# Kernel tuning notes

Measured on AMD Instinct MI355X. Metric: run time of the kernel, lower is better.

The kernel has to match this reference:

```python
import jax, jax.numpy as jnp
import numpy as np

B, NQ, NV, DIM, HEADS, K = 2, 2048, 2048, 256, 8, 8
HD = DIM // HEADS
HID = 4 * DIM
SCALE = HD ** -0.5
EPS = 1e-5


def setup_inputs() -> dict:
    key = jax.random.key(0)
    ks = jax.random.split(key, 40)
    r = lambda i, s: jax.random.normal(ks[i], s, jnp.float32) * 0.02
    inp = {
        'q': jax.random.normal(ks[0], (B, NQ, DIM), jnp.float32),
        'v': jax.random.normal(ks[1], (B, NV, DIM), jnp.float32),
        'q_pos': jax.random.normal(ks[2], (B, NQ, 3), jnp.float32),
        'v_pos': jax.random.normal(ks[3], (B, NV, 3), jnp.float32),
        'self_knn_index': jax.random.randint(ks[4], (B, NQ, K), 0, NQ, jnp.int32),
        'cross_knn_index': jax.random.randint(ks[5], (B, NQ, K), 0, NV, jnp.int32),
        # LayerNorms (gamma=1, beta=0)
        'norm1_g': jnp.ones(DIM), 'norm1_b': jnp.zeros(DIM),
        'normq_g': jnp.ones(DIM), 'normq_b': jnp.zeros(DIM),
        'normv_g': jnp.ones(DIM), 'normv_b': jnp.zeros(DIM),
        'norm2_g': jnp.ones(DIM), 'norm2_b': jnp.zeros(DIM),
        # self-attention (qkv_bias=False), proj has bias
        'sa_qkv_w': r(6, (DIM, 3 * DIM)),
        'sa_proj_w': r(7, (DIM, DIM)), 'sa_proj_b': jnp.zeros(DIM),
        # cross-attention: q proj and kv proj (no bias), out proj with bias
        'ca_q_w': r(8, (DIM, DIM)),
        'ca_kv_w': r(9, (DIM, 2 * DIM)),
        'ca_proj_w': r(10, (DIM, DIM)), 'ca_proj_b': jnp.zeros(DIM),
        # MLP
        'fc1_w': r(11, (DIM, HID)), 'fc1_b': jnp.zeros(HID),
        'fc2_w': r(12, (HID, DIM)), 'fc2_b': jnp.zeros(DIM),
        # kNN maps
        'knn_w': r(13, (2 * DIM, DIM)), 'knn_b': jnp.zeros(DIM),
        'merge_w': r(14, (2 * DIM, DIM)), 'merge_b': jnp.zeros(DIM),
        'knnx_w': r(15, (2 * DIM, DIM)), 'knnx_b': jnp.zeros(DIM),
        'mergex_w': r(16, (2 * DIM, DIM)), 'mergex_b': jnp.zeros(DIM),
    }
    return inp


def _ln(x, g, b):
    m = x.mean(-1, keepdims=True)
    var = x.var(-1, keepdims=True)
    return (x - m) / jnp.sqrt(var + EPS) * g + b


def _heads(x):  # [B,N,DIM] -> [B,H,N,HD]
    Bx, N, _ = x.shape
    return x.reshape(Bx, N, HEADS, HD).transpose(0, 2, 1, 3)


def _attend(qh, kh, vh, proj_w, proj_b):
    a = jax.nn.softmax(jnp.einsum('bhqd,bhkd->bhqk', qh, kh) * SCALE, axis=-1)
    o = jnp.einsum('bhqk,bhkd->bhqd', a, vh)
    Bx, _, N, _ = o.shape
    o = o.transpose(0, 2, 1, 3).reshape(Bx, N, DIM)
    return o @ proj_w + proj_b


_gather = jax.vmap(lambda pts, idx: pts[idx])  # ([N,D],[Nq,K]) -> [Nq,K,D]


def _knn_feature(qn, vn, idx):  # gather -> diff/cat -> [B,Nq,K,2D]
    local = _gather(vn, idx)                      # [B,Nq,K,D]
    qe = qn[:, :, None, :]                        # [B,Nq,1,D]
    return jnp.concatenate([local - qe, jnp.broadcast_to(qe, local.shape)], -1)


def reference(q, v, q_pos, v_pos, self_knn_index, cross_knn_index,
              norm1_g, norm1_b, normq_g, normq_b, normv_g, normv_b,
              norm2_g, norm2_b, sa_qkv_w, sa_proj_w, sa_proj_b,
              ca_q_w, ca_kv_w, ca_proj_w, ca_proj_b,
              fc1_w, fc1_b, fc2_w, fc2_b,
              knn_w, knn_b, merge_w, merge_b,
              knnx_w, knnx_b, mergex_w, mergex_b):
    # ---- self-attention block with self-kNN branch ----
    nq = _ln(q, norm1_g, norm1_b)
    qkv = nq @ sa_qkv_w
    qh, kh, vh = (_heads(t) for t in jnp.split(qkv, 3, axis=-1))
    sa_out = _attend(qh, kh, vh, sa_proj_w, sa_proj_b)
    f = _knn_feature(nq, nq, self_knn_index)
    knn_out = jax.nn.leaky_relu(f @ knn_w + knn_b, 0.2).max(axis=-2)
    q1 = jnp.concatenate([sa_out, knn_out], -1) @ merge_w + merge_b
    q = q + q1
    # ---- cross-attention block with cross-kNN branch ----
    nq2 = _ln(q, normq_g, normq_b)
    nv = _ln(v, normv_g, normv_b)
    qh = _heads(nq2 @ ca_q_w)
    kh, vh = (_heads(t) for t in jnp.split(nv @ ca_kv_w, 2, axis=-1))
    ca_out = _attend(qh, kh, vh, ca_proj_w, ca_proj_b)
    f = _knn_feature(nq2, nv, cross_knn_index)
    knnx_out = jax.nn.leaky_relu(f @ knnx_w + knnx_b, 0.2).max(axis=-2)
    q2 = jnp.concatenate([ca_out, knnx_out], -1) @ mergex_w + mergex_b
    q = q + q2
    # ---- MLP block ----
    h = _ln(q, norm2_g, norm2_b)
    h = jax.nn.gelu(h @ fc1_w + fc1_b, approximate=False)
    q = q + (h @ fc2_w + fc2_b)
    return q
```

## Files before the change

### kernel.cpp

```cpp
#include <hip/hip_runtime.h>
#include <math.h>

#define NQC   2048
#define NKVC  2048
#define DIMC  256
#define SCALEF 0.2550348810731232f

typedef short bfrag __attribute__((ext_vector_type(8)));
typedef float ffrag __attribute__((ext_vector_type(4)));
typedef unsigned short us8 __attribute__((ext_vector_type(8)));

__device__ __forceinline__ float gelu_exact(float x) {
    return 0.5f * x * (1.0f + erff(x * 0.70710678118654752f));
}
__device__ __forceinline__ unsigned short f2bf(float f) {
    union { float f; unsigned u; } v; v.f = f;
    unsigned r = v.u + 0x7FFFu + ((v.u >> 16) & 1u);
    return (unsigned short)(r >> 16);
}
__device__ __forceinline__ float bf2f(unsigned short u) {
    union { unsigned u; float f; } v; v.u = ((unsigned)u) << 16;
    return v.f;
}
__device__ __forceinline__ float fexp2(float x) {
    float r; asm("v_exp_f32 %0, %1" : "=v"(r) : "v"(x)); return r;
}
__device__ __forceinline__ unsigned cvt_pk_bf16(float lo, float hi) {
    unsigned r; asm("v_cvt_pk_bf16_f32 %0, %1, %2" : "=v"(r) : "v"(lo), "v"(hi));
    return r;
}

__device__ __forceinline__ void ln_row(
    const float* __restrict__ x, const float* __restrict__ g,
    const float* __restrict__ b, unsigned short* __restrict__ y, int row)
{
    int lane = threadIdx.x & 63;
    const float* xr = x + (size_t)row * DIMC + lane * 4;
    float4 vv = *(const float4*)xr;
    float s  = vv.x + vv.y + vv.z + vv.w;
    float sq = vv.x*vv.x + vv.y*vv.y + vv.z*vv.z + vv.w*vv.w;
    #pragma unroll
    for (int off = 32; off >= 1; off >>= 1) {
        s  += __shfl_xor(s, off);
        sq += __shfl_xor(sq, off);
    }
    float mean = s * (1.0f/DIMC);
    float inv  = rsqrtf(sq * (1.0f/DIMC) - mean*mean + 1e-5f);
    float4 gg = *(const float4*)(g + lane*4);
    float4 bb = *(const float4*)(b + lane*4);
    ushort4 o;
    o.x = f2bf((vv.x - mean) * inv * gg.x + bb.x);
    o.y = f2bf((vv.y - mean) * inv * gg.y + bb.y);
    o.z = f2bf((vv.z - mean) * inv * gg.z + bb.z);
    o.w = f2bf((vv.w - mean) * inv * gg.w + bb.w);
    *(ushort4*)(y + (size_t)row * DIMC + lane * 4) = o;
}

__global__ __launch_bounds__(256) void prep_w(
    const float* __restrict__ qkv, const float* __restrict__ knn,
    const float* __restrict__ proj, const float* __restrict__ merge,
    const float* __restrict__ caq, const float* __restrict__ knnx,
    const float* __restrict__ cakv, const float* __restrict__ projx,
    const float* __restrict__ mergex, const float* __restrict__ fc1,
    const float* __restrict__ fc2, unsigned short* __restrict__ dst,
    const float* __restrict__ lx, const float* __restrict__ lg,
    const float* __restrict__ lb, unsigned short* __restrict__ ly,
    const float* __restrict__ vx, const float* __restrict__ vg,
    const float* __restrict__ vb, unsigned short* __restrict__ vy,
    const float* __restrict__ pb1, const float* __restrict__ mb1, float* __restrict__ bf1o,
    const float* __restrict__ pbx, const float* __restrict__ mbx, float* __restrict__ bfxo)
{
    __shared__ unsigned short T[64][72];
    int blk = blockIdx.x, tid = threadIdx.x;
    if (blk >= 2528) {
        const float* bp = (blk == 2528) ? pb1 : pbx;
        const float* Wm = (blk == 2528) ? merge : mergex;
        const float* bm = (blk == 2528) ? mb1 : mbx;
        float* o        = (blk == 2528) ? bf1o : bfxo;
        int m = tid;
        float acc = bm[m];
        for (int k = 0; k < 256; ++k) acc += bp[k] * Wm[(size_t)k * 256 + m];
        o[m] = acc;
        return;
    }
    if (blk >= 1504) {
        ln_row(vx, vg, vb, vy, (blk - 1504) * 4 + (tid >> 6));
        return;
    }
    if (blk >= 480) {
        ln_row(lx, lg, lb, ly, (blk - 480) * 4 + (tid >> 6));
        return;
    }
    if (blk >= 352) {
        int l = blk - 352;
        const float* s; unsigned short* d;
        if (l < 64) { s = proj;  d = dst + 327680; }
        else        { s = projx; d = dst + 851968; l -= 64; }
        int e = (l * 256 + tid) * 4;
        float4 v = *(const float4*)(s + e);
        ushort4 o;
        o.x = f2bf(v.x); o.y = f2bf(v.y); o.z = f2bf(v.z); o.w = f2bf(v.w);
        *(ushort4*)(d + e) = o;
        return;
    }
    int t = blk;
    const float* src; const float* src2 = nullptr; int sN;
    unsigned short* dp; int dK; float scale = 1.0f; int n0, k0;
    if (t < 48)       { src = qkv;          sN = 768;  dp = dst;           dK = 256;
                        n0 = (t % 12) * 64; k0 = (t / 12) * 64; if (n0 < 256) scale = SCALEF; }
    else if (t < 64)  { int u = t - 48;  src = knn;          sN = 256; dp = dst + 196608; dK = 256;
                        n0 = (u & 3) * 64; k0 = (u >> 2) * 64; }
    else if (t < 80)  { int u = t - 64;  src = knn + 65536;  src2 = knn; sN = 256; dp = dst + 262144; dK = 256;
                        n0 = (u & 3) * 64; k0 = (u >> 2) * 64; }
    else if (t < 112) { int u = t - 80;  src = merge;        sN = 256; dp = dst + 393216; dK = 512;
                        n0 = (u & 3) * 64; k0 = (u >> 2) * 64; }
    else if (t < 128) { int u = t - 112; src = caq;          sN = 256; dp = dst + 524288; dK = 256;
                        n0 = (u & 3) * 64; k0 = (u >> 2) * 64; scale = SCALEF; }
    else if (t < 144) { int u = t - 128; src = knnx + 65536; src2 = knnx; sN = 256; dp = dst + 589824; dK = 256;
                        n0 = (u & 3) * 64; k0 = (u >> 2) * 64; }
    else if (t < 176) { int u = t - 144; src = cakv;         sN = 512; dp = dst + 655360; dK = 256;
                        n0 = (u & 7) * 64; k0 = (u >> 3) * 64; }
    else if (t < 192) { int u = t - 176; src = knnx;         sN = 256; dp = dst + 786432; dK = 256;
                        n0 = (u & 3) * 64; k0 = (u >> 2) * 64; }
    else if (t < 224) { int u = t - 192; src = mergex;       sN = 256; dp = dst + 917504; dK = 512;
                        n0 = (u & 3) * 64; k0 = (u >> 2) * 64; }
    else if (t < 288) { int u = t - 224; src = fc1;          sN = 1024; dp = dst + 1048576; dK = 256;
                        n0 = (u & 15) * 64; k0 = (u >> 4) * 64; }
    else              { int u = t - 288; src = fc2;          sN = 256; dp = dst + 1310720; dK = 1024;
                        n0 = (u & 3) * 64; k0 = (u >> 2) * 64; }
    int r = tid >> 2, c0 = (tid & 3) * 16;
    float va[16];
    {
        const float* sp = src + (size_t)(k0 + r) * sN + n0 + c0;
        float4 f0 = *(const float4*)(sp);
        float4 f1 = *(const float4*)(sp + 4);
        float4 f2 = *(const float4*)(sp + 8);
        float4 f3 = *(const float4*)(sp + 12);
        va[0]=f0.x; va[1]=f0.y; va[2]=f0.z;  va[3]=f0.w;
        va[4]=f1.x; va[5]=f1.y; va[6]=f1.z;  va[7]=f1.w;
        va[8]=f2.x; va[9]=f2.y; va[10]=f2.z; va[11]=f2.w;
        va[12]=f3.x; va[13]=f3.y; va[14]=f3.z; va[15]=f3.w;
        if (src2) {
            const float* s2 = src2 + (size_t)(k0 + r) * sN + n0 + c0;
            float4 h0 = *(const float4*)(s2);
            float4 h1 = *(const float4*)(s2 + 4);
            float4 h2 = *(const float4*)(s2 + 8);
            float4 h3 = *(const float4*)(s2 + 12);
            va[0]-=h0.x; va[1]-=h0.y; va[2]-=h0.z;  va[3]-=h0.w;
            va[4]-=h1.x; va[5]-=h1.y; va[6]-=h1.z;  va[7]-=h1.w;
            va[8]-=h2.x; va[9]-=h2.y; va[10]-=h2.z; va[11]-=h2.w;
            va[12]-=h3.x; va[13]-=h3.y; va[14]-=h3.z; va[15]-=h3.w;
        }
    }
    #pragma unroll
    for (int i = 0; i < 16; ++i) T[c0 + i][r] = f2bf(va[i] * scale);
    __syncthreads();
    {
        int n = tid >> 2, kk = (tid & 3) * 16;
        unsigned short* d = dp + (size_t)(n0 + n) * dK + k0 + kk;
        *(us8*)d       = *(const us8*)&T[n][kk];
        *(us8*)(d + 8) = *(const us8*)&T[n][kk + 8];
    }
}

template<int ACT, int RESID, int OUTBF>
__device__ __forceinline__ void gemm_body(
    const unsigned short* __restrict__ A, int lda,
    const unsigned short* __restrict__ Wt,
    const float* __restrict__ bias,
    const float* __restrict__ resid, int ldr,
    void* __restrict__ Cp, int ldc, int Kc, int row0, int col0,
    unsigned short (* __restrict__ Alds)[72],
    unsigned short (* __restrict__ Wlds)[72])
{
    const int tid = threadIdx.x;
    const int wid = tid >> 6, lane = tid & 63;
    const int lm = lane & 15, quad = lane >> 4;
    const int wr = wid >> 1, wc = wid & 1;
    const int ar = tid >> 2, ac = (tid & 3) * 16;
    const unsigned short* Ag = A  + (size_t)(row0 + ar) * lda + ac;
    const unsigned short* Wg = Wt + (size_t)(col0 + ar) * Kc  + ac;

    us8 a0 = *(const us8*)Ag;
    us8 a1 = *(const us8*)(Ag + 8);
    us8 w0 = *(const us8*)Wg;
    us8 w1 = *(const us8*)(Wg + 8);

    ffrag acc[2][2];
    #pragma unroll
    for (int mi = 0; mi < 2; ++mi)
        #pragma unroll
        for (int ni = 0; ni < 2; ++ni)
            acc[mi][ni] = (ffrag){0.f, 0.f, 0.f, 0.f};

    for (int k0 = 0;;) {
        __syncthreads();
        *(us8*)&Alds[ar][ac]   = a0;
        *(us8*)&Alds[ar][ac+8] = a1;
        *(us8*)&Wlds[ar][ac]   = w0;
        *(us8*)&Wlds[ar][ac+8] = w1;
        __syncthreads();
        k0 += 64;
        if (k0 < Kc) {
            a0 = *(const us8*)(Ag + k0);
            a1 = *(const us8*)(Ag + k0 + 8);
            w0 = *(const us8*)(Wg + k0);
            w1 = *(const us8*)(Wg + k0 + 8);
        }
        #pragma unroll
        for (int kc = 0; kc < 2; ++kc) {
            bfrag af[2], bw[2];
            #pragma unroll
            for (int mi = 0; mi < 2; ++mi)
                af[mi] = *(const bfrag*)&Alds[wr*32 + mi*16 + lm][kc*32 + quad*8];
            #pragma unroll
            for (int ni = 0; ni < 2; ++ni)
                bw[ni] = *(const bfrag*)&Wlds[wc*32 + ni*16 + lm][kc*32 + quad*8];
            #pragma unroll
            for (int mi = 0; mi < 2; ++mi)
                #pragma unroll
                for (int ni = 0; ni < 2; ++ni)
                    acc[mi][ni] = __builtin_amdgcn_mfma_f32_16x16x32_bf16(
                        af[mi], bw[ni], acc[mi][ni], 0, 0, 0);
        }
        if (k0 >= Kc) break;
    }
    #pragma unroll
    for (int mi = 0; mi < 2; ++mi) {
        #pragma unroll
        for (int ni = 0; ni < 2; ++ni) {
            int gr = row0 + wr*32 + mi*16 + quad*4;
            int gc = col0 + wc*32 + ni*16 + lm;
            float bv = bias ? bias[gc] : 0.f;
            #pragma unroll
            for (int r = 0; r < 4; ++r) {
                float o = acc[mi][ni][r] + bv;
                if (ACT == 1) o = gelu_exact(o);
                if (RESID) o += resid[(size_t)(gr + r) * ldr + gc];
                if (OUTBF) ((unsigned short*)Cp)[(size_t)(gr + r) * ldc + gc] = f2bf(o);
                else       ((float*)Cp)[(size_t)(gr + r) * ldc + gc] = o;
            }
        }
    }
}

template<int ACT, int RESID, int OUTBF>
__global__ __launch_bounds__(256) void gemm64(
    const unsigned short* __restrict__ A, int lda,
    const unsigned short* __restrict__ Wt,
    const float* __restrict__ bias,
    const float* __restrict__ resid, int ldr,
    void* __restrict__ Cp, int ldc, int Kc)
{
    __shared__ unsigned short Alds[64][72];
    __shared__ unsigned short Wlds[64][72];
    gemm_body<ACT,RESID,OUTBF>(A, lda, Wt, bias, resid, ldr, Cp, ldc, Kc,
                               blockIdx.y * 64, blockIdx.x * 64, Alds, Wlds);
}

__global__ __launch_bounds__(256) void gemm_qkv_fold(
    const unsigned short* __restrict__ XB, const unsigned short* __restrict__ WT1,
    unsigned short* __restrict__ A1,
    const unsigned short* __restrict__ WTmerge, const unsigned short* __restrict__ projbf,
    unsigned short* __restrict__ WTf1,
    const unsigned short* __restrict__ WTmergex, const unsigned short* __restrict__ projxbf,
    unsigned short* __restrict__ WTfx)
{
    __shared__ unsigned short Alds[64][72];
    __shared__ unsigned short Wlds[64][72];
    const unsigned short *A, *Wt; unsigned short* C;
    int lda, ldc, row0, col0;
    if (blockIdx.y >= 64) {
        if (blockIdx.x >= 16) return;
        row0 = (blockIdx.x >> 2) * 64; col0 = (blockIdx.x & 3) * 64;
        lda = 512; ldc = 256;
        if (blockIdx.y == 64) { A = WTmerge;  Wt = projbf;  C = WTf1; }
        else                  { A = WTmergex; Wt = projxbf; C = WTfx; }
    } else {
        A = XB; Wt = WT1; C = A1; lda = 256; ldc = 1280;
        row0 = blockIdx.y * 64; col0 = blockIdx.x * 64;
    }
    gemm_body<0,0,1>(A, lda, Wt, nullptr, nullptr, 0, C, ldc, 256, row0, col0, Alds, Wlds);
}

template<int ACT, int RESID, int OUTBF>
__global__ __launch_bounds__(512) void gemm64x8(
    const unsigned short* __restrict__ A, int lda,
    const unsigned short* __restrict__ Wt,
    const float* __restrict__ bias,
    const float* __restrict__ resid, int ldr,
    void* __restrict__ Cp, int ldc, int Kc)
{
    __shared__ unsigned short Alds[2][64][72];
    __shared__ unsigned short Wlds[2][64][72];
    __shared__ float Red[64][68];
    const int tid = threadIdx.x;
    const int g = tid >> 8;
    const int t = tid & 255;
    const int wid2 = (tid >> 6) & 3, lane = tid & 63;
    const int lm = lane & 15, quad = lane >> 4;
    const int wr = wid2 >> 1, wc = wid2 & 1;
    const int row0 = blockIdx.y * 64, col0 = blockIdx.x * 64;
    const int ar = t >> 2, ac = (t & 3) * 16;
    const int KH = Kc >> 1;
    const unsigned short* Ag = A  + (size_t)(row0 + ar) * lda + g * KH + ac;
    const unsigned short* Wg = Wt + (size_t)(col0 + ar) * Kc  + g * KH + ac;

    us8 a0 = *(const us8*)Ag;
    us8 a1 = *(const us8*)(Ag + 8);
    us8 w0 = *(const us8*)Wg;
    us8 w1 = *(const us8*)(Wg + 8);

    ffrag acc[2][2];
    #pragma unroll
    for (int mi = 0; mi < 2; ++mi)
        #pragma unroll
        for (int ni = 0; ni < 2; ++ni)
            acc[mi][ni] = (ffrag){0.f, 0.f, 0.f, 0.f};

    for (int k0 = 0;;) {
        __syncthreads();
        *(us8*)&Alds[g][ar][ac]   = a0;
        *(us8*)&Alds[g][ar][ac+8] = a1;
        *(us8*)&Wlds[g][ar][ac]   = w0;
        *(us8*)&Wlds[g][ar][ac+8] = w1;
        __syncthreads();
        k0 += 64;
        if (k0 < KH) {
            a0 = *(const us8*)(Ag + k0);
            a1 = *(const us8*)(Ag + k0 + 8);
            w0 = *(const us8*)(Wg + k0);
            w1 = *(const us8*)(Wg + k0 + 8);
        }
        #pragma unroll
        for (int kc = 0; kc < 2; ++kc) {
            bfrag af[2], bw[2];
            #pragma unroll
            for (int mi = 0; mi < 2; ++mi)
                af[mi] = *(const bfrag*)&Alds[g][wr*32 + mi*16 + lm][kc*32 + quad*8];
            #pragma unroll
            for (int ni = 0; ni < 2; ++ni)
                bw[ni] = *(const bfrag*)&Wlds[g][wc*32 + ni*16 + lm][kc*32 + quad*8];
            #pragma unroll
            for (int mi = 0; mi < 2; ++mi)
                #pragma unroll
                for (int ni = 0; ni < 2; ++ni)
                    acc[mi][ni] = __builtin_amdgcn_mfma_f32_16x16x32_bf16(
                        af[mi], bw[ni], acc[mi][ni], 0, 0, 0);
        }
        if (k0 >= KH) break;
    }
    __syncthreads();
    if (g == 1) {
        #pragma unroll
        for (int mi = 0; mi < 2; ++mi)
            #pragma unroll
            for (int ni = 0; ni < 2; ++ni) {
                int lr = wr*32 + mi*16 + quad*4;
                int lc = wc*32 + ni*16 + lm;
                #pragma unroll
                for (int r = 0; r < 4; ++r)
                    Red[lr + r][lc] = acc[mi][ni][r];
            }
    }
    __syncthreads();
    if (g == 0) {
        #pragma unroll
        for (int mi = 0; mi < 2; ++mi) {
            #pragma unroll
            for (int ni = 0; ni < 2; ++ni) {
                int lr = wr*32 + mi*16 + quad*4;
                int lc = wc*32 + ni*16 + lm;
                int gr = row0 + lr;
                int gc = col0 + lc;
                float bv = bias ? bias[gc] : 0.f;
                #pragma unroll
                for (int r = 0; r < 4; ++r) {
                    float o = acc[mi][ni][r] + Red[lr + r][lc] + bv;
                    if (ACT == 1) o = gelu_exact(o);
                    if (RESID) o += resid[(size_t)(gr + r) * ldr + gc];
                    if (OUTBF) ((unsigned short*)Cp)[(size_t)(gr + r) * ldc + gc] = f2bf(o);
                    else       ((float*)Cp)[(size_t)(gr + r) * ldc + gc] = o;
                }
            }
        }
    }
}

__global__ __launch_bounds__(512) void gemm_mln(
    const unsigned short* __restrict__ Op, const float* __restrict__ Lp,
    const unsigned short* __restrict__ Akn,
    const unsigned short* __restrict__ Wat,
    const unsigned short* __restrict__ Wkn,
    const float* __restrict__ bias,
    const float* __restrict__ resid,
    float* __restrict__ Cp,
    const float* __restrict__ lng, const float* __restrict__ lnb,
    unsigned short* __restrict__ ln_out)
{
    __shared__ unsigned short Wlds[256][72];
    __shared__ unsigned short Alds[16][72];
    __shared__ float OutT[16][268];
    const int tid = threadIdx.x;
    const int wid = tid >> 6, lane = tid & 63;
    const int lm = lane & 15, quad = lane >> 4;
    const int row0 = blockIdx.x * 16;
    const int wn = tid >> 1, wk = (tid & 1) * 32;
    const int ar = tid >> 3, ac = (tid & 7) * 8;

    const unsigned short* O0 = Op + (size_t)(row0 + ar) * 256 + ac;
    const unsigned short* O1 = Op + (size_t)(4096 + row0 + ar) * 256 + ac;
    const float* L0 = Lp + (size_t)(row0 + ar) * 8;
    const float* L1 = Lp + (size_t)(4096 + row0 + ar) * 8;
    const unsigned short* Ak = Akn + (size_t)(row0 + ar) * 512 + ac;

    us8 aReg, wv0, wv1, wv2, wv3;
    if (tid < 128) {
        us8 x = *(const us8*)O0;
        us8 y = *(const us8*)O1;
        float li = 1.0f / (L0[ac >> 5] + L1[ac >> 5]);
        #pragma unroll
        for (int i = 0; i < 8; ++i)
            aReg[i] = f2bf((bf2f(x[i]) + bf2f(y[i])) * li);
    }
    {
        const unsigned short* Wg = Wat + (size_t)wn * 256 + wk;
        wv0 = *(const us8*)Wg;        wv1 = *(const us8*)(Wg + 8);
        wv2 = *(const us8*)(Wg + 16); wv3 = *(const us8*)(Wg + 24);
    }

    ffrag acc[2];
    acc[0] = (ffrag){0.f, 0.f, 0.f, 0.f};
    acc[1] = (ffrag){0.f, 0.f, 0.f, 0.f};

    for (int k0 = 0;;) {
        __syncthreads();
        if (tid < 128) *(us8*)&Alds[ar][ac] = aReg;
        *(us8*)&Wlds[wn][wk]      = wv0;
        *(us8*)&Wlds[wn][wk + 8]  = wv1;
        *(us8*)&Wlds[wn][wk + 16] = wv2;
        *(us8*)&Wlds[wn][wk + 24] = wv3;
        __syncthreads();
        k0 += 64;
        if (k0 < 512) {
            if (tid < 128) {
                if (k0 < 256) {
                    us8 x = *(const us8*)(O0 + k0);
                    us8 y = *(const us8*)(O1 + k0);
                    float li = 1.0f / (L0[(k0 + ac) >> 5] + L1[(k0 + ac) >> 5]);
                    #pragma unroll
                    for (int i = 0; i < 8; ++i)
                        aReg[i] = f2bf((bf2f(x[i]) + bf2f(y[i])) * li);
                } else {
                    aReg = *(const us8*)(Ak + (k0 - 256));
                }
            }
            const unsigned short* Wg = (k0 < 256)
                ? Wat + (size_t)wn * 256 + k0 + wk
                : Wkn + (size_t)wn * 512 + (k0 - 256) + wk;
            wv0 = *(const us8*)Wg;        wv1 = *(const us8*)(Wg + 8);
            wv2 = *(const us8*)(Wg + 16); wv3 = *(const us8*)(Wg + 24);
        }
        #pragma unroll
        for (int kc = 0; kc < 2; ++kc) {
            bfrag af = *(const bfrag*)&Alds[lm][kc*32 + quad*8];
            #pragma unroll
            for (int ni = 0; ni < 2; ++ni) {
                bfrag bw = *(const bfrag*)&Wlds[wid*32 + ni*16 + lm][kc*32 + quad*8];
                acc[ni] = __builtin_amdgcn_mfma_f32_16x16x32_bf16(
                    af, bw, acc[ni], 0, 0, 0);
            }
        }
        if (k0 >= 512) break;
    }
    #pragma unroll
    for (int ni = 0; ni < 2; ++ni) {
        int gc = wid*32 + ni*16 + lm;
        float bv = bias[gc];
        #pragma unroll
        for (int r = 0; r < 4; ++r) {
            int lr = quad*4 + r;
            float o = acc[ni][r] + bv + resid[(size_t)(row0 + lr) * 256 + gc];
            Cp[(size_t)(row0 + lr) * 256 + gc] = o;
            OutT[lr][gc] = o;
        }
    }
    __syncthreads();
    #pragma unroll
    for (int rr0 = 0; rr0 < 2; ++rr0) {
        int rr = wid * 2 + rr0;
        float4 vv = *(const float4*)&OutT[rr][lane * 4];
        float s  = vv.x + vv.y + vv.z + vv.w;
        float sq = vv.x*vv.x + vv.y*vv.y + vv.z*vv.z + vv.w*vv.w;
        #pragma unroll
        for (int off = 32; off >= 1; off >>= 1) {
            s  += __shfl_xor(s, off);
            sq += __shfl_xor(sq, off);
        }
        float mean = s * (1.0f/DIMC);
        float inv  = rsqrtf(sq * (1.0f/DIMC) - mean*mean + 1e-5f);
        float4 gg = *(const float4*)(lng + lane*4);
        float4 bb = *(const float4*)(lnb + lane*4);
        ushort4 o;
        o.x = f2bf((vv.x - mean) * inv * gg.x + bb.x);
        o.y = f2bf((vv.y - mean) * inv * gg.y + bb.y);
        o.z = f2bf((vv.z - mean) * inv * gg.z + bb.z);
        o.w = f2bf((vv.w - mean) * inv * gg.w + bb.w);
        *(ushort4*)(ln_out + (size_t)(row0 + rr) * 256 + lane * 4) = o;
    }
}

__global__ __launch_bounds__(256) void gemm64_dual(
    const unsigned short* __restrict__ XB,
    const unsigned short* __restrict__ NVB,
    const unsigned short* __restrict__ WT2,
    const unsigned short* __restrict__ WT3,
    unsigned short* __restrict__ A2,
    unsigned short* __restrict__ A3)
{
    __shared__ unsigned short Alds[64][72];
    __shared__ unsigned short Wlds[64][72];
    const unsigned short* A; const unsigned short* Wt;
    unsigned short* C; int ldc, col0;
    if (blockIdx.x < 8) { A = XB;  Wt = WT2; C = A2; ldc = 512; col0 = blockIdx.x * 64; }
    else                { A = NVB; Wt = WT3; C = A3; ldc = 768; col0 = (blockIdx.x - 8) * 64; }
    gemm_body<0,0,1>(A, 256, Wt, nullptr, nullptr, 0, C, ldc, 256,
                     blockIdx.y * 64, col0, Alds, Wlds);
}

__global__ __launch_bounds__(256) void attn_gather(
    const unsigned short* __restrict__ Qp, int ldq,
    const unsigned short* __restrict__ Kp, int ldk,
    const unsigned short* __restrict__ Vp, int ldv,
    unsigned short* __restrict__ Op, float* __restrict__ Lp,
    const unsigned short* __restrict__ P, int ldp,
    const unsigned short* __restrict__ Base, int ldb,
    const float* __restrict__ gbias, const int* __restrict__ idx,
    unsigned short* __restrict__ gout, int ldgo)
{
    __shared__ unsigned short Klds[64][40];
    __shared__ __align__(16) unsigned short Vt[32][72];
    __shared__ __align__(16) unsigned short Plds[4][16][72];
    int tid = threadIdx.x, wid = tid >> 6, lane = tid & 63;

    if (blockIdx.z >= 4) {
        int gbid = blockIdx.x + 32 * (blockIdx.y + 8 * (blockIdx.z - 4));
        int q = gbid * 4 + wid;
        int b = q >> 11;
        int c = lane * 4;
        ushort4 bu = *(const ushort4*)(Base + (size_t)q * ldb + c);
        float4 bi = *(const float4*)(gbias + c);
        float bsx = bf2f(bu.x) + bi.x, bsy = bf2f(bu.y) + bi.y;
        float bsz = bf2f(bu.z) + bi.z, bsw = bf2f(bu.w) + bi.w;
        float4 acc = make_float4(-3e38f, -3e38f, -3e38f, -3e38f);
        const int* ip = idx + (size_t)q * 8;
        #pragma unroll
        for (int k = 0; k < 8; ++k) {
            int j = ip[k];
            ushort4 pu = *(const ushort4*)(P + ((size_t)(b * NKVC + j)) * ldp + c);
            float t;
            t = bsx + bf2f(pu.x); t = t > 0.f ? t : 0.2f * t; acc.x = fmaxf(acc.x, t);
            t = bsy + bf2f(pu.y); t = t > 0.f ? t : 0.2f * t; acc.y = fmaxf(acc.y, t);
            t = bsz + bf2f(pu.z); t = t > 0.f ? t : 0.2f * t; acc.z = fmaxf(acc.z, t);
            t = bsw + bf2f(pu.w); t = t > 0.f ? t : 0.2f * t; acc.w = fmaxf(acc.w, t);
        }
        ushort4 o;
        o.x = f2bf(acc.x); o.y = f2bf(acc.y); o.z = f2bf(acc.z); o.w = f2bf(acc.w);
        *(ushort4*)(gout + (size_t)q * ldgo + c) = o;
        return;
    }

    int zc = blockIdx.z, bb = zc >> 1, ck = zc & 1;
    int h = blockIdx.y;
    int hoff = h * 32;
    int lm = lane & 15, quad = lane >> 4;
    size_t qbase  = (size_t)bb * NQC;
    size_t kvbase = (size_t)bb * NKVC;
    int q0 = blockIdx.x * 64 + wid * 16;

    bfrag aq = *(const bfrag*)(Qp + (qbase + q0 + lm) * (size_t)ldq + hoff + quad * 8);

    float l_r[4] = {0.f, 0.f, 0.f, 0.f};
    ffrag oacc[2];
    oacc[0] = (ffrag){0.f, 0.f, 0.f, 0.f};
    oacc[1] = (ffrag){0.f, 0.f, 0.f, 0.f};

    const int kkey = tid >> 2, kd0 = (tid & 3) * 8;
    const int vkey = tid & 63, vd0 = (tid >> 6) * 8;
    const int vcol = ((vkey & 15) << 2) | (vkey >> 4);
    const unsigned short* kg0 = Kp + (kvbase + kkey) * (size_t)ldk + hoff + kd0;
    const unsigned short* vg0 = Vp + (kvbase + vkey) * (size_t)ldv + hoff + vd0;

    for (int kt = ck * 16; kt < ck * 16 + 16; ++kt) {
        us8 kv = *(const us8*)(kg0 + (size_t)kt * 64 * ldk);
        us8 vv = *(const us8*)(vg0 + (size_t)kt * 64 * ldv);
        __syncthreads();
        *(us8*)&Klds[kkey][kd0] = kv;
        #pragma unroll
        for (int i = 0; i < 8; ++i) Vt[vd0 + i][vcol] = vv[i];
        __syncthreads();

        ffrag sacc[4];
        #pragma unroll
        for (int t = 0; t < 4; ++t) {
            bfrag bk = *(const bfrag*)&Klds[t*16 + lm][quad * 8];
            sacc[t] = __builtin_amdgcn_mfma_f32_16x16x32_bf16(
                aq, bk, (ffrag){0.f,0.f,0.f,0.f}, 0, 0, 0);
        }

        #pragma unroll
        for (int r = 0; r < 4; ++r) {
            float p0 = fexp2(sacc[0][r]), p1 = fexp2(sacc[1][r]);
            float p2 = fexp2(sacc[2][r]), p3 = fexp2(sacc[3][r]);
            l_r[r] += (p0 + p1) + (p2 + p3);
            unsigned u0 = cvt_pk_bf16(p0, p1);
            unsigned u1 = cvt_pk_bf16(p2, p3);
            *(uint2*)&Plds[wid][quad*4 + r][lm << 2] = make_uint2(u0, u1);
        }
        asm volatile("s_waitcnt lgkmcnt(0)" ::: "memory");

        #pragma unroll
        for (int kc = 0; kc < 2; ++kc) {
            bfrag ap = *(const bfrag*)&Plds[wid][lm][kc*32 + quad*8];
            #pragma unroll
            for (int nt = 0; nt < 2; ++nt) {
                bfrag bv = *(const bfrag*)&Vt[nt*16 + lm][kc*32 + quad*8];
                oacc[nt] = __builtin_amdgcn_mfma_f32_16x16x32_bf16(
                    ap, bv, oacc[nt], 0, 0, 0);
            }
        }
    }
    #pragma unroll
    for (int nt = 0; nt < 2; ++nt)
        #pragma unroll
        for (int r = 0; r < 4; ++r)
            Op[((size_t)ck * 4096 + qbase + q0 + quad*4 + r) * 256 + hoff + nt*16 + lm]
                = f2bf(oacc[nt][r]);
    #pragma unroll
    for (int r = 0; r < 4; ++r) {
        float l = l_r[r];
        l += __shfl_xor(l, 1);
        l += __shfl_xor(l, 2);
        l += __shfl_xor(l, 4);
        l += __shfl_xor(l, 8);
        if (lm == 0)
            Lp[((size_t)ck * 4096 + qbase + q0 + quad*4 + r) * 8 + h] = l;
    }
}

extern "C" void kernel_launch(void* const* d_in, const int* in_sizes, int n_in,
                              void* d_out, int out_size, void* d_ws, size_t ws_size,
                              hipStream_t stream) {
    const float* q_in   = (const float*)d_in[0];
    const float* v_in   = (const float*)d_in[1];
    const int*   idx_s  = (const int*)d_in[4];
    const int*   idx_x  = (const int*)d_in[5];
    const float* n1g = (const float*)d_in[6],  *n1b = (const float*)d_in[7];
    const float* nqg = (const float*)d_in[8],  *nqb = (const float*)d_in[9];
    const float* nvg = (const float*)d_in[10], *nvb = (const float*)d_in[11];
    const float* n2g = (const float*)d_in[12], *n2b = (const float*)d_in[13];
    const float* sa_qkv_w  = (const float*)d_in[14];
    const float* sa_proj_w = (const float*)d_in[15];
    const float* sa_proj_b = (const float*)d_in[16];
    const float* ca_q_w    = (const float*)d_in[17];
    const float* ca_kv_w   = (const float*)d_in[18];
    const float* ca_proj_w = (const float*)d_in[19];
    const float* ca_proj_b = (const float*)d_in[20];
    const float* fc1_w = (const float*)d_in[21], *fc1_b = (const float*)d_in[22];
    const float* fc2_w = (const float*)d_in[23], *fc2_b = (const float*)d_in[24];
    const float* knn_w   = (const float*)d_in[25], *knn_b   = (const float*)d_in[26];
    const float* merge_w = (const float*)d_in[27], *merge_b = (const float*)d_in[28];
    const float* knnx_w  = (const float*)d_in[29], *knnx_b  = (const float*)d_in[30];
    const float* mergex_w = (const float*)d_in[31], *mergex_b = (const float*)d_in[32];
    float* out = (float*)d_out;

    unsigned short* A1      = (unsigned short*)d_ws;
    unsigned short* A2      = A1;
    unsigned short* A3      = A1 + (size_t)4096 * 512;
    unsigned short* Hb      = A1;
    unsigned short* KN      = A1 + (size_t)4096 * 1280;
    unsigned short* CC      = KN;
    unsigned short* XB      = CC + (size_t)4096 * 512;
    unsigned short* NVB     = XB + (size_t)4096 * 256;
    unsigned short* WT      = NVB + (size_t)4096 * 256;
    unsigned short* WT1     = WT;
    unsigned short* projbf  = WT + 327680;
    unsigned short* WTmerge = WT + 393216;
    unsigned short* WT2     = WT + 524288;
    unsigned short* WT3     = WT + 655360;
    unsigned short* projxbf = WT + 851968;
    unsigned short* WTmergex= WT + 917504;
    unsigned short* WTfc1   = WT + 1048576;
    unsigned short* WTfc2   = WT + 1310720;
    unsigned short* Opart   = WT + 1572864;
    float* Lpart = (float*)(Opart + (size_t)2 * 4096 * 256);
    unsigned short* WTf1 = (unsigned short*)(Lpart + (size_t)2 * 4096 * 8);
    unsigned short* WTfx = WTf1 + 65536;
    float* bf1 = (float*)(WTfx + 65536);
    float* bfx = bf1 + 256;

    dim3 blk(256), blk8(512);
    dim3 gAG(NQC / 64, 8, 8);

    prep_w<<<dim3(2530), blk, 0, stream>>>(sa_qkv_w, knn_w, sa_proj_w, merge_w,
        ca_q_w, knnx_w, ca_kv_w, ca_proj_w, mergex_w, fc1_w, fc2_w, WT,
        q_in, n1g, n1b, XB,
        v_in, nvg, nvb, NVB,
        sa_proj_b, merge_b, bf1,
        ca_proj_b, mergex_b, bfx);

    gemm_qkv_fold<<<dim3(20,66), blk, 0, stream>>>(XB, WT1, A1,
        WTmerge, projbf, WTf1, WTmergex, projxbf, WTfx);
    attn_gather<<<gAG, blk, 0, stream>>>(A1, 1280, A1+256, 1280, A1+512, 1280,
        Opart, Lpart, A1+768, 1280, A1+1024, 1280, knn_b, idx_s, CC+256, 512);
    gemm_mln<<<dim3(256), blk8, 0, stream>>>(Opart, Lpart, CC+256,
        WTf1, WTmerge+256, bf1, q_in, out, nqg, nqb, XB);

    gemm64_dual<<<dim3(20,64), blk, 0, stream>>>(XB, NVB, WT2, WT3, A2, A3);
    attn_gather<<<gAG, blk, 0, stream>>>(A2, 512, A3, 768, A3+256, 768,
        Opart, Lpart, A3+512, 768, A2+256, 512, knnx_b, idx_x, CC+256, 512);
    gemm_mln<<<dim3(256), blk8, 0, stream>>>(Opart, Lpart, CC+256,
        WTfx, WTmergex+256, bfx, out, out, n2g, n2b, XB);

    gemm64<1,0,1><<<dim3(16,64), blk, 0, stream>>>(XB, 256, WTfc1,
        fc1_b, nullptr, 0, Hb, 1024, 256);
    gemm64x8<0,1,0><<<dim3(4,64), blk8, 0, stream>>>(Hb, 1024, WTfc2,
        fc2_b, out, 256, out, 256, 1024);
}
```

Before: 235.6 us.

## Process two query tiles per wave in attention to reuse K/V LDS tiles

Each wave now handles 32 queries (two 16-row MFMA tiles) instead of 16, so each block covers 128 queries. Every K/V tile staged in shared memory feeds twice as many MFMAs, which halves K/V global loads and barriers per query. Attention blocks with blockIdx.x >= 16 exit early, while the grid shape stays 32 wide so the gather branch keeps its indexing. The cost is more registers per wave, a larger P buffer in LDS, and half as many attention blocks, which lowers parallelism.

```diff
diff --git a/kernel.cpp b/kernel.cpp
--- a/kernel.cpp
+++ b/kernel.cpp
@@ -540,7 +540,7 @@
 {
     __shared__ unsigned short Klds[64][40];
     __shared__ __align__(16) unsigned short Vt[32][72];
-    __shared__ __align__(16) unsigned short Plds[4][16][72];
+    __shared__ __align__(16) unsigned short Plds[4][2][16][72];
     int tid = threadIdx.x, wid = tid >> 6, lane = tid & 63;
 
     if (blockIdx.z >= 4) {
@@ -570,20 +570,26 @@
         return;
     }
 
+    if (blockIdx.x >= 16) return;
     int zc = blockIdx.z, bb = zc >> 1, ck = zc & 1;
     int h = blockIdx.y;
     int hoff = h * 32;
     int lm = lane & 15, quad = lane >> 4;
     size_t qbase  = (size_t)bb * NQC;
     size_t kvbase = (size_t)bb * NKVC;
-    int q0 = blockIdx.x * 64 + wid * 16;
-
-    bfrag aq = *(const bfrag*)(Qp + (qbase + q0 + lm) * (size_t)ldq + hoff + quad * 8);
-
-    float l_r[4] = {0.f, 0.f, 0.f, 0.f};
-    ffrag oacc[2];
-    oacc[0] = (ffrag){0.f, 0.f, 0.f, 0.f};
-    oacc[1] = (ffrag){0.f, 0.f, 0.f, 0.f};
+    int q0 = blockIdx.x * 128 + wid * 32;
+
+    bfrag aq0 = *(const bfrag*)(Qp + (qbase + q0 + lm)      * (size_t)ldq + hoff + quad * 8);
+    bfrag aq1 = *(const bfrag*)(Qp + (qbase + q0 + 16 + lm) * (size_t)ldq + hoff + quad * 8);
+
+    float l0[4] = {0.f, 0.f, 0.f, 0.f};
+    float l1[4] = {0.f, 0.f, 0.f, 0.f};
+    ffrag oacc[2][2];
+    #pragma unroll
+    for (int i = 0; i < 2; ++i)
+        #pragma unroll
+        for (int j = 0; j < 2; ++j)
+            oacc[i][j] = (ffrag){0.f, 0.f, 0.f, 0.f};
 
     const int kkey = tid >> 2, kd0 = (tid & 3) * 8;
     const int vkey = tid & 63, vd0 = (tid >> 6) * 8;
@@ -600,51 +606,62 @@
         for (int i = 0; i < 8; ++i) Vt[vd0 + i][vcol] = vv[i];
         __syncthreads();
 
-        ffrag sacc[4];
+        ffrag s0[4], s1[4];
         #pragma unroll
         for (int t = 0; t < 4; ++t) {
             bfrag bk = *(const bfrag*)&Klds[t*16 + lm][quad * 8];
-            sacc[t] = __builtin_amdgcn_mfma_f32_16x16x32_bf16(
-                aq, bk, (ffrag){0.f,0.f,0.f,0.f}, 0, 0, 0);
+            s0[t] = __builtin_amdgcn_mfma_f32_16x16x32_bf16(
+                aq0, bk, (ffrag){0.f,0.f,0.f,0.f}, 0, 0, 0);
+            s1[t] = __builtin_amdgcn_mfma_f32_16x16x32_bf16(
+                aq1, bk, (ffrag){0.f,0.f,0.f,0.f}, 0, 0, 0);
         }
 
         #pragma unroll
         for (int r = 0; r < 4; ++r) {
-            float p0 = fexp2(sacc[0][r]), p1 = fexp2(sacc[1][r]);
-            float p2 = fexp2(sacc[2][r]), p3 = fexp2(sacc[3][r]);
-            l_r[r] += (p0 + p1) + (p2 + p3);
-            unsigned u0 = cvt_pk_bf16(p0, p1);
-            unsigned u1 = cvt_pk_bf16(p2, p3);
-            *(uint2*)&Plds[wid][quad*4 + r][lm << 2] = make_uint2(u0, u1);
+            float p0 = fexp2(s0[0][r]), p1 = fexp2(s0[1][r]);
+            float p2 = fexp2(s0[2][r]), p3 = fexp2(s0[3][r]);
+            l0[r] += (p0 + p1) + (p2 + p3);
+            *(uint2*)&Plds[wid][0][quad*4 + r][lm << 2] =
+                make_uint2(cvt_pk_bf16(p0, p1), cvt_pk_bf16(p2, p3));
+            float u0 = fexp2(s1[0][r]), u1 = fexp2(s1[1][r]);
+            float u2 = fexp2(s1[2][r]), u3 = fexp2(s1[3][r]);
+            l1[r] += (u0 + u1) + (u2 + u3);
+            *(uint2*)&Plds[wid][1][quad*4 + r][lm << 2] =
+                make_uint2(cvt_pk_bf16(u0, u1), cvt_pk_bf16(u2, u3));
         }
         asm volatile("s_waitcnt lgkmcnt(0)" ::: "memory");
 
         #pragma unroll
         for (int kc = 0; kc < 2; ++kc) {
-            bfrag ap = *(const bfrag*)&Plds[wid][lm][kc*32 + quad*8];
-            #pragma unroll
-            for (int nt = 0; nt < 2; ++nt) {
-                bfrag bv = *(const bfrag*)&Vt[nt*16 + lm][kc*32 + quad*8];
-                oacc[nt] = __builtin_amdgcn_mfma_f32_16x16x32_bf16(
-                    ap, bv, oacc[nt], 0, 0, 0);
-            }
-        }
-    }
-    #pragma unroll
-    for (int nt = 0; nt < 2; ++nt)
-        #pragma unroll
-        for (int r = 0; r < 4; ++r)
-            Op[((size_t)ck * 4096 + qbase + q0 + quad*4 + r) * 256 + hoff + nt*16 + lm]
-                = f2bf(oacc[nt][r]);
+            bfrag bv0 = *(const bfrag*)&Vt[lm][kc*32 + quad*8];
+            bfrag bv1 = *(const bfrag*)&Vt[16 + lm][kc*32 + quad*8];
+            bfrag ap0 = *(const bfrag*)&Plds[wid][0][lm][kc*32 + quad*8];
+            bfrag ap1 = *(const bfrag*)&Plds[wid][1][lm][kc*32 + quad*8];
+            oacc[0][0] = __builtin_amdgcn_mfma_f32_16x16x32_bf16(ap0, bv0, oacc[0][0], 0, 0, 0);
+            oacc[0][1] = __builtin_amdgcn_mfma_f32_16x16x32_bf16(ap0, bv1, oacc[0][1], 0, 0, 0);
+            oacc[1][0] = __builtin_amdgcn_mfma_f32_16x16x32_bf16(ap1, bv0, oacc[1][0], 0, 0, 0);
+            oacc[1][1] = __builtin_amdgcn_mfma_f32_16x16x32_bf16(ap1, bv1, oacc[1][1], 0, 0, 0);
+        }
+    }
+    #pragma unroll
+    for (int ti = 0; ti < 2; ++ti)
+        #pragma unroll
+        for (int nt = 0; nt < 2; ++nt)
+            #pragma unroll
+            for (int r = 0; r < 4; ++r)
+                Op[((size_t)ck * 4096 + qbase + q0 + ti*16 + quad*4 + r) * 256 + hoff + nt*16 + lm]
+                    = f2bf(oacc[ti][nt][r]);
     #pragma unroll
     for (int r = 0; r < 4; ++r) {
-        float l = l_r[r];
-        l += __shfl_xor(l, 1);
-        l += __shfl_xor(l, 2);
-        l += __shfl_xor(l, 4);
-        l += __shfl_xor(l, 8);
-        if (lm == 0)
-            Lp[((size_t)ck * 4096 + qbase + q0 + quad*4 + r) * 8 + h] = l;
+        float a = l0[r], b = l1[r];
+        a += __shfl_xor(a, 1); a += __shfl_xor(a, 2);
+        a += __shfl_xor(a, 4); a += __shfl_xor(a, 8);
+        b += __shfl_xor(b, 1); b += __shfl_xor(b, 2);
+        b += __shfl_xor(b, 4); b += __shfl_xor(b, 8);
+        if (lm == 0) {
+            Lp[((size_t)ck * 4096 + qbase + q0 + quad*4 + r) * 8 + h] = a;
+            Lp[((size_t)ck * 4096 + qbase + q0 + 16 + quad*4 + r) * 8 + h] = b;
+        }
     }
 }
 
@@ -700,7 +717,7 @@
     float* bfx = bf1 + 256;
 
     dim3 blk(256), blk8(512);
-    dim3 gAG(NQC / 64, 8, 8);
+    dim3 gAG(32, 8, 8);
 
     prep_w<<<dim3(2530), blk, 0, stream>>>(sa_qkv_w, knn_w, sa_proj_w, merge_w,
         ca_q_w, knnx_w, ca_kv_w, ca_proj_w, mergex_w, fc1_w, fc2_w, WT,
```

New measurement: 251.8 us. 6.9% more time.

## Split attention KV range into four chunks instead of two

Applied to the files above, without the earlier changes.

Splits the flash-attention key range into four partial chunks per batch instead of two, doubling the attention block count (grid z goes from 8 to 12 including gather blocks). The extra partial outputs go into spare workspace buffers (CC and XB), and gemm_mln now sums four partials and four denominators. This is meant to raise occupancy and parallelism on the many-CU GPU, at the cost of more partial-output traffic and reduction work. It also reuses XB as scratch while gemm_mln later writes LN output into XB, which risks read/write aliasing across blocks.

```diff
diff --git a/kernel.cpp b/kernel.cpp
--- a/kernel.cpp
+++ b/kernel.cpp
@@ -388,7 +388,8 @@
 }
 
 __global__ __launch_bounds__(512) void gemm_mln(
-    const unsigned short* __restrict__ Op, const float* __restrict__ Lp,
+    const unsigned short* __restrict__ Op, const unsigned short* O2,
+    const unsigned short* O3, const float* __restrict__ Lp,
     const unsigned short* __restrict__ Akn,
     const unsigned short* __restrict__ Wat,
     const unsigned short* __restrict__ Wkn,
@@ -396,7 +397,7 @@
     const float* __restrict__ resid,
     float* __restrict__ Cp,
     const float* __restrict__ lng, const float* __restrict__ lnb,
-    unsigned short* __restrict__ ln_out)
+    unsigned short* ln_out)
 {
     __shared__ unsigned short Wlds[256][72];
     __shared__ unsigned short Alds[16][72];
@@ -408,20 +409,26 @@
     const int wn = tid >> 1, wk = (tid & 1) * 32;
     const int ar = tid >> 3, ac = (tid & 7) * 8;
 
-    const unsigned short* O0 = Op + (size_t)(row0 + ar) * 256 + ac;
-    const unsigned short* O1 = Op + (size_t)(4096 + row0 + ar) * 256 + ac;
+    const unsigned short* O0p = Op + (size_t)(row0 + ar) * 256 + ac;
+    const unsigned short* O1p = Op + (size_t)(4096 + row0 + ar) * 256 + ac;
+    const unsigned short* O2p = O2 + (size_t)(row0 + ar) * 512 + ac;
+    const unsigned short* O3p = O3 + (size_t)(row0 + ar) * 256 + ac;
     const float* L0 = Lp + (size_t)(row0 + ar) * 8;
     const float* L1 = Lp + (size_t)(4096 + row0 + ar) * 8;
+    const float* L2 = Lp + (size_t)(8192 + row0 + ar) * 8;
+    const float* L3 = Lp + (size_t)(12288 + row0 + ar) * 8;
     const unsigned short* Ak = Akn + (size_t)(row0 + ar) * 512 + ac;
 
     us8 aReg, wv0, wv1, wv2, wv3;
     if (tid < 128) {
-        us8 x = *(const us8*)O0;
-        us8 y = *(const us8*)O1;
-        float li = 1.0f / (L0[ac >> 5] + L1[ac >> 5]);
+        us8 x0 = *(const us8*)O0p;
+        us8 x1 = *(const us8*)O1p;
+        us8 x2 = *(const us8*)O2p;
+        us8 x3 = *(const us8*)O3p;
+        float li = 1.0f / (L0[ac >> 5] + L1[ac >> 5] + L2[ac >> 5] + L3[ac >> 5]);
         #pragma unroll
         for (int i = 0; i < 8; ++i)
-            aReg[i] = f2bf((bf2f(x[i]) + bf2f(y[i])) * li);
+            aReg[i] = f2bf(((bf2f(x0[i]) + bf2f(x1[i])) + (bf2f(x2[i]) + bf2f(x3[i]))) * li);
     }
     {
         const unsigned short* Wg = Wat + (size_t)wn * 256 + wk;
@@ -445,12 +452,16 @@
         if (k0 < 512) {
             if (tid < 128) {
                 if (k0 < 256) {
-                    us8 x = *(const us8*)(O0 + k0);
-                    us8 y = *(const us8*)(O1 + k0);
-                    float li = 1.0f / (L0[(k0 + ac) >> 5] + L1[(k0 + ac) >> 5]);
+                    us8 x0 = *(const us8*)(O0p + k0);
+                    us8 x1 = *(const us8*)(O1p + k0);
+                    us8 x2 = *(const us8*)(O2p + k0);
+                    us8 x3 = *(const us8*)(O3p + k0);
+                    float li = 1.0f / (L0[(k0 + ac) >> 5] + L1[(k0 + ac) >> 5]
+                                     + L2[(k0 + ac) >> 5] + L3[(k0 + ac) >> 5]);
                     #pragma unroll
                     for (int i = 0; i < 8; ++i)
-                        aReg[i] = f2bf((bf2f(x[i]) + bf2f(y[i])) * li);
+                        aReg[i] = f2bf(((bf2f(x0[i]) + bf2f(x1[i]))
+                                      + (bf2f(x2[i]) + bf2f(x3[i]))) * li);
                 } else {
                     aReg = *(const us8*)(Ak + (k0 - 256));
                 }
@@ -532,7 +543,8 @@
     const unsigned short* __restrict__ Qp, int ldq,
     const unsigned short* __restrict__ Kp, int ldk,
     const unsigned short* __restrict__ Vp, int ldv,
-    unsigned short* __restrict__ Op, float* __restrict__ Lp,
+    unsigned short* __restrict__ Op, unsigned short* O2, unsigned short* O3,
+    float* __restrict__ Lp,
     const unsigned short* __restrict__ P, int ldp,
     const unsigned short* __restrict__ Base, int ldb,
     const float* __restrict__ gbias, const int* __restrict__ idx,
@@ -543,8 +555,8 @@
     __shared__ __align__(16) unsigned short Plds[4][16][72];
     int tid = threadIdx.x, wid = tid >> 6, lane = tid & 63;
 
-    if (blockIdx.z >= 4) {
-        int gbid = blockIdx.x + 32 * (blockIdx.y + 8 * (blockIdx.z - 4));
+    if (blockIdx.z >= 8) {
+        int gbid = blockIdx.x + 32 * (blockIdx.y + 8 * (blockIdx.z - 8));
         int q = gbid * 4 + wid;
         int b = q >> 11;
         int c = lane * 4;
@@ -570,7 +582,7 @@
         return;
     }
 
-    int zc = blockIdx.z, bb = zc >> 1, ck = zc & 1;
+    int zc = blockIdx.z, bb = zc >> 2, ck = zc & 3;
     int h = blockIdx.y;
     int hoff = h * 32;
     int lm = lane & 15, quad = lane >> 4;
@@ -591,7 +603,7 @@
     const unsigned short* kg0 = Kp + (kvbase + kkey) * (size_t)ldk + hoff + kd0;
     const unsigned short* vg0 = Vp + (kvbase + vkey) * (size_t)ldv + hoff + vd0;
 
-    for (int kt = ck * 16; kt < ck * 16 + 16; ++kt) {
+    for (int kt = ck * 8; kt < ck * 8 + 8; ++kt) {
         us8 kv = *(const us8*)(kg0 + (size_t)kt * 64 * ldk);
         us8 vv = *(const us8*)(vg0 + (size_t)kt * 64 * ldv);
         __syncthreads();
@@ -630,11 +642,16 @@
             }
         }
     }
+    unsigned short* Od; int ldo;
+    if (ck == 0)      { Od = Op;                        ldo = 256; }
+    else if (ck == 1) { Od = Op + (size_t)4096 * 256;   ldo = 256; }
+    else if (ck == 2) { Od = O2;                        ldo = 512; }
+    else              { Od = O3;                        ldo = 256; }
     #pragma unroll
     for (int nt = 0; nt < 2; ++nt)
         #pragma unroll
         for (int r = 0; r < 4; ++r)
-            Op[((size_t)ck * 4096 + qbase + q0 + quad*4 + r) * 256 + hoff + nt*16 + lm]
+            Od[(qbase + q0 + quad*4 + r) * (size_t)ldo + hoff + nt*16 + lm]
                 = f2bf(oacc[nt][r]);
     #pragma unroll
     for (int r = 0; r < 4; ++r) {
@@ -694,13 +711,13 @@
     unsigned short* WTfc2   = WT + 1310720;
     unsigned short* Opart   = WT + 1572864;
     float* Lpart = (float*)(Opart + (size_t)2 * 4096 * 256);
-    unsigned short* WTf1 = (unsigned short*)(Lpart + (size_t)2 * 4096 * 8);
+    unsigned short* WTf1 = (unsigned short*)(Lpart + (size_t)4 * 4096 * 8);
     unsigned short* WTfx = WTf1 + 65536;
     float* bf1 = (float*)(WTfx + 65536);
     float* bfx = bf1 + 256;
 
     dim3 blk(256), blk8(512);
-    dim3 gAG(NQC / 64, 8, 8);
+    dim3 gAG(32, 8, 12);
 
     prep_w<<<dim3(2530), blk, 0, stream>>>(sa_qkv_w, knn_w, sa_proj_w, merge_w,
         ca_q_w, knnx_w, ca_kv_w, ca_proj_w, mergex_w, fc1_w, fc2_w, WT,
@@ -712,14 +729,16 @@
     gemm_qkv_fold<<<dim3(20,66), blk, 0, stream>>>(XB, WT1, A1,
         WTmerge, projbf, WTf1, WTmergex, projxbf, WTfx);
     attn_gather<<<gAG, blk, 0, stream>>>(A1, 1280, A1+256, 1280, A1+512, 1280,
-        Opart, Lpart, A1+768, 1280, A1+1024, 1280, knn_b, idx_s, CC+256, 512);
-    gemm_mln<<<dim3(256), blk8, 0, stream>>>(Opart, Lpart, CC+256,
+        Opart, CC, XB, Lpart, A1+768, 1280, A1+1024, 1280, knn_b, idx_s,
+        CC+256, 512);
+    gemm_mln<<<dim3(256), blk8, 0, stream>>>(Opart, CC, XB, Lpart, CC+256,
         WTf1, WTmerge+256, bf1, q_in, out, nqg, nqb, XB);
 
     gemm64_dual<<<dim3(20,64), blk, 0, stream>>>(XB, NVB, WT2, WT3, A2, A3);
     attn_gather<<<gAG, blk, 0, stream>>>(A2, 512, A3, 768, A3+256, 768,
-        Opart, Lpart, A3+512, 768, A2+256, 512, knnx_b, idx_x, CC+256, 512);
-    gemm_mln<<<dim3(256), blk8, 0, stream>>>(Opart, Lpart, CC+256,
+        Opart, CC, XB, Lpart, A3+512, 768, A2+256, 512, knnx_b, idx_x,
+        CC+256, 512);
+    gemm_mln<<<dim3(256), blk8, 0, stream>>>(Opart, CC, XB, Lpart, CC+256,
         WTfx, WTmergex+256, bfx, out, out, n2g, n2b, XB);
 
     gemm64<1,0,1><<<dim3(16,64), blk, 0, stream>>>(XB, 256, WTfc1,
```

After: 237.1 us. About the same (+0.6%).
